# Kernel optimization log

Measured on AMD Instinct MI355X. Metric: run time of the kernel, lower is better.

## Reference

```python
import jax, jax.numpy as jnp
import numpy as np

N, E, DIN, DH, R = 50000, 1600000, 128, 128, 3


def setup_inputs() -> dict:
    key = jax.random.key(0)
    ks = jax.random.split(key, 32)
    inp = {}
    inp["x"] = jax.random.normal(ks[0], (N, DIN), jnp.float32)
    inp["h_prev"] = jax.random.normal(ks[1], (N, DH), jnp.float32)
    inp["edge_index"] = jax.random.randint(ks[2], (2, E), 0, N)
    inp["node_role"] = jax.random.randint(ks[3], (N,), 0, R)
    i = 4
    for name, din, has_b in (("xz", DIN, True), ("hz", DH, False), ("xr", DIN, True), ("hr", DH, False), ("xh", DIN, True), ("hh", DH, False)):
        inp[name + "_W"] = jax.random.normal(ks[i], (din, DH), jnp.float32) / np.float32(np.sqrt(din)); i += 1
        inp[name + "_Wg"] = jax.random.normal(ks[i], (R, DH), jnp.float32) * np.float32(0.1); i += 1
        inp[name + "_bg"] = jnp.zeros((R, DH), jnp.float32)
        inp[name + "_S"] = jax.random.normal(ks[i], (R, DH, DH), jnp.float32) / np.float32(np.sqrt(DH)); i += 1
        if has_b:
            inp[name + "_b"] = jnp.zeros((R, DH), jnp.float32)
    return inp


def _role_conv(x, W, Wg, bg, S, b, row, col, node_role):
    # x: [N, din] -> transformed features [N, DH]
    xt = x @ W
    r = node_role[row]                                  # role of source node per edge
    g = jax.nn.sigmoid(Wg[r] + bg[r])                   # [Etot, DH] role gate
    msg = xt[row] * g
    if b is not None:
        msg = msg + b[r]
    n = x.shape[0]
    summed = jax.ops.segment_sum(msg, col, num_segments=n)
    cnt = jax.ops.segment_sum(jnp.ones((row.shape[0],), xt.dtype), col, num_segments=n)
    aggr = summed / jnp.maximum(cnt, 1.0)[:, None]      # scatter_mean (self-loops ensure cnt>=1)
    # per-role self transform: out[i] = xt[i] @ S[role[i]] + aggr[i]
    out = aggr
    for nr in range(R):
        out = out + jnp.where((node_role == nr)[:, None], xt @ S[nr], jnp.float32(0.0))
    return jax.nn.relu(out)


def reference(x, edge_index, h_prev, node_role,
              xz_W, xz_Wg, xz_bg, xz_S, xz_b,
              hz_W, hz_Wg, hz_bg, hz_S,
              xr_W, xr_Wg, xr_bg, xr_S, xr_b,
              hr_W, hr_Wg, hr_bg, hr_S,
              xh_W, xh_Wg, xh_bg, xh_S, xh_b,
              hh_W, hh_Wg, hh_bg, hh_S):
    n = x.shape[0]
    loops = jnp.arange(n, dtype=edge_index.dtype)
    row = jnp.concatenate([edge_index[0], loops])       # add_self_loops appended at end
    col = jnp.concatenate([edge_index[1], loops])

    z = jax.nn.sigmoid(_role_conv(x, xz_W, xz_Wg, xz_bg, xz_S, xz_b, row, col, node_role)
                       + _role_conv(h_prev, hz_W, hz_Wg, hz_bg, hz_S, None, row, col, node_role))
    r = jax.nn.sigmoid(_role_conv(x, xr_W, xr_Wg, xr_bg, xr_S, xr_b, row, col, node_role)
                       + _role_conv(h_prev, hr_W, hr_Wg, hr_bg, hr_S, None, row, col, node_role))
    h_tilde = jnp.tanh(_role_conv(x, xh_W, xh_Wg, xh_bg, xh_S, xh_b, row, col, node_role)
                       + _role_conv(r * h_prev, hh_W, hh_Wg, hh_bg, hh_S, None, row, col, node_role))
    h_new = z * h_prev + (1.0 - z) * h_tilde
    return h_new
```

## Files before the change

### kernel.cpp

```cpp
#include <hip/hip_runtime.h>


typedef __bf16 bf16;
typedef __bf16 bf16x8 __attribute__((ext_vector_type(8)));
typedef float  f32x4  __attribute__((ext_vector_type(4)));
typedef float  f32x2  __attribute__((ext_vector_type(2)));
typedef unsigned char u8;

#define DH 128

__device__ __forceinline__ float sigmoidf_(float x) { return 1.0f / (1.0f + expf(-x)); }

__global__ __launch_bounds__(256) void hist_kernel(const int* __restrict__ ei, const int* __restrict__ role,
                                                   int* __restrict__ cnt3, int* __restrict__ rolecnt,
                                                   int E, int N)
{
  int i = blockIdx.x * 256 + threadIdx.x;
  int lane = threadIdx.x & 63;
  int r = (i < N) ? role[i] : -1;
  #pragma unroll
  for (int rr = 0; rr < 3; ++rr) {
    unsigned long long mask = __ballot(r == rr);
    if (lane == 0 && mask) atomicAdd(&rolecnt[rr], __popcll(mask));
  }
  if (i < E + N) {
    int src, dst;
    if (i < E) { src = ei[i]; dst = ei[E + i]; } else { src = i - E; dst = i - E; }
    int rs = (i < E) ? role[src] : r;
    if (i >= E) rs = role[i - E];
    atomicAdd(&cnt3[dst * 3 + rs], 1);
  }
}

__global__ __launch_bounds__(1024) void scan1_kernel(const int* __restrict__ cnt, int* __restrict__ off,
                                                     int* __restrict__ bsum, int n)
{
  __shared__ int wsum[16];
  int t = threadIdx.x, lane = t & 63, w = t >> 6;
  int idx = blockIdx.x * 1024 + t;
  int v = (idx < n) ? cnt[idx] : 0;
  int s = v;
  #pragma unroll
  for (int d = 1; d < 64; d <<= 1) { int u = __shfl_up(s, d); if (lane >= d) s += u; }
  if (lane == 63) wsum[w] = s;
  __syncthreads();
  if (w == 0 && lane < 16) {
    int ws = wsum[lane];
    #pragma unroll
    for (int d = 1; d < 16; d <<= 1) { int u = __shfl_up(ws, d); if (lane >= d) ws += u; }
    wsum[lane] = ws;
  }
  __syncthreads();
  int inc = ((w > 0) ? wsum[w - 1] : 0) + s;
  if (idx < n) off[idx + 1] = inc;
  if (t == 1023) bsum[blockIdx.x] = inc;
}

__global__ void scan2_kernel(int* __restrict__ bsum, int nb, const int* __restrict__ rolecnt,
                             int* __restrict__ rolefill, int* __restrict__ roleinfo)
{
  int lane = threadIdx.x;
  int carry = 0;
  for (int base = 0; base < nb; base += 64) {
    int v = (base + lane < nb) ? bsum[base + lane] : 0;
    int s = v;
    #pragma unroll
    for (int d = 1; d < 64; d <<= 1) { int u = __shfl_up(s, d); if (lane >= d) s += u; }
    if (base + lane < nb) bsum[base + lane] = carry + s - v;
    carry += __shfl(s, 63);
  }
  if (lane == 0) {
    int c0 = rolecnt[0], c1 = rolecnt[1], c2 = rolecnt[2];
    int s1 = (c0 + 255) & ~255;
    int s2 = s1 + ((c1 + 255) & ~255);
    int mp = s2 + ((c2 + 255) & ~255);
    rolefill[0] = 0; rolefill[1] = s1; rolefill[2] = s2;
    roleinfo[0] = s1; roleinfo[1] = s2;
    roleinfo[2] = c0;      roleinfo[3] = s1 - c0;
    roleinfo[4] = s1 + c1; roleinfo[5] = s2 - s1 - c1;
    roleinfo[6] = s2 + c2; roleinfo[7] = mp - s2 - c2;
  }
}

__global__ __launch_bounds__(1024) void scan3_kernel(int* __restrict__ off, int* __restrict__ fill,
                                                     const int* __restrict__ bsum, int n)
{
  int idx = blockIdx.x * 1024 + threadIdx.x;
  if (idx == 0) { off[0] = 0; fill[0] = 0; }
  if (idx < n) {
    int v = off[idx + 1] + bsum[blockIdx.x];
    off[idx + 1] = v;
    if (idx + 1 < n) fill[idx + 1] = v;
  }
}

__global__ __launch_bounds__(256) void scatter_kernel(const int* __restrict__ ei, const int* __restrict__ spos,
                                                      const int* __restrict__ roleinfo,
                                                      int* __restrict__ fill3, int* __restrict__ ssrc, int E, int N)
{
  int i = blockIdx.x * 256 + threadIdx.x;
  if (i >= E + N) return;
  int s1 = roleinfo[0], s2 = roleinfo[1];
  int src, dst;
  if (i < E) { src = ei[i]; dst = ei[E + i]; } else { src = i - E; dst = i - E; }
  int t = spos[src];
  int r = (t >= s2) ? 2 : (t >= s1) ? 1 : 0;
  int pz = atomicAdd(&fill3[dst * 3 + r], 1);
  ssrc[pz] = t;
}

__global__ __launch_bounds__(256) void permscatter_kernel(const int* __restrict__ role, int* __restrict__ rolefill,
                                                          int* __restrict__ spos, int* __restrict__ sposinv, int N)
{
  int i = blockIdx.x * 256 + threadIdx.x;
  int lane = threadIdx.x & 63;
  int r = (i < N) ? role[i] : -1;
  #pragma unroll
  for (int rr = 0; rr < 3; ++rr) {
    unsigned long long mask = __ballot(r == rr);
    if (!mask) continue;
    int base = 0;
    if (lane == 0) base = atomicAdd(&rolefill[rr], __popcll(mask));
    base = __shfl(base, 0);
    if (r == rr) {
      int rank = (int)__popcll(mask & ((1ull << lane) - 1ull));
      int pos = base + rank;
      spos[i] = pos;
      sposinv[pos] = i;
    }
  }
}

__global__ __launch_bounds__(256) void zeropad_kernel(const int* __restrict__ roleinfo,
                                                      bf16* __restrict__ Ax, bf16* __restrict__ Ah)
{
  int id = blockIdx.x * 256 + threadIdx.x;
  int a = id / 49152, rem = id % 49152;
  int gp = rem / 16384, r2 = rem % 16384;
  int rr = r2 >> 6, c = r2 & 63;
  int gs = roleinfo[2 + gp * 2], gl = roleinfo[3 + gp * 2];
  if (rr < gl) {
    int row = gs + rr;
    size_t unit = (size_t)(row >> 4) * 1024 + c * 16 + (row & 15);
    bf16x8 z = {};
    ((bf16x8*)(a == 0 ? Ax : Ah))[unit] = z;
  }
}

__global__ __launch_bounds__(256) void prep_xh_kernel(const float* __restrict__ x, const float* __restrict__ h,
                                                      const int* __restrict__ spos, u8* __restrict__ xq8,
                                                      bf16* __restrict__ Ax, bf16* __restrict__ Ah, int N)
{
  int g = blockIdx.x * 256 + threadIdx.x;
  if (g >= N * 32) return;
  int n = g >> 5, j = g & 31;
  int t = spos[n];
  const float* src = (j < 16) ? (x + (size_t)n * 128 + (j << 3))
                              : (h + (size_t)n * 128 + ((j - 16) << 3));
  float4 v0 = ((const float4*)src)[0];
  float4 v1 = ((const float4*)src)[1];
  int lo = __builtin_amdgcn_cvt_pk_fp8_f32(v0.x, v0.y, 0, false);
  lo = __builtin_amdgcn_cvt_pk_fp8_f32(v0.z, v0.w, lo, true);
  int hi = __builtin_amdgcn_cvt_pk_fp8_f32(v1.x, v1.y, 0, false);
  hi = __builtin_amdgcn_cvt_pk_fp8_f32(v1.z, v1.w, hi, true);
  *(int2*)(xq8 + (size_t)t * 256 + j * 8) = make_int2(lo, hi);
  bf16x8 o;
  o[0] = (bf16)v0.x; o[1] = (bf16)v0.y; o[2] = (bf16)v0.z; o[3] = (bf16)v0.w;
  o[4] = (bf16)v1.x; o[5] = (bf16)v1.y; o[6] = (bf16)v1.z; o[7] = (bf16)v1.w;
  size_t unit = (size_t)(t >> 4) * 1024 + (48 + (j & 15)) * 16 + (t & 15);
  ((bf16x8*)(j < 16 ? Ax : Ah))[unit] = o;
}

struct PrepW { const float* W[6]; const float* Wg[6]; const float* bg[6]; };
__global__ __launch_bounds__(256) void prep_wf_kernel(PrepW pw, bf16* __restrict__ Wf)
{
  int idx = blockIdx.x * 256 + threadIdx.x;
  if (idx >= 294912) return;
  int cv = idx / 49152, pos = idx % 49152;
  int ks4q = pos >> 10;
  int col = (pos >> 3) & 127, j = pos & 7;
  int k = (ks4q >> 2) * 32 + (ks4q & 3) * 8 + j;
  int r = k >> 7, kk = k & 127;
  float g = sigmoidf_(pw.Wg[cv][r * 128 + col] + pw.bg[cv][r * 128 + col]);
  Wf[idx] = (bf16)(pw.W[cv][kk * 128 + col] * g);
}

struct PrepP { const float* W[6]; const float* S[6]; };
__global__ __launch_bounds__(128) void prep_pf_kernel(PrepP pp, bf16* __restrict__ Pf)
{
  int b = blockIdx.x;
  int cv = b / 384, rem = b % 384;
  int r = rem >> 7, kp = rem & 127;
  int col = threadIdx.x;
  const float* W = pp.W[cv] + (size_t)kp * 128;
  const float* S = pp.S[cv] + (size_t)r * 16384;
  float sum = 0.f;
  #pragma unroll 4
  for (int j2 = 0; j2 < 128; ++j2) sum += W[j2] * S[j2 * 128 + col];
  size_t o = (size_t)(cv * 3 + r) * 16384 + ((size_t)(kp >> 3) * 128 + col) * 8 + (kp & 7);
  Pf[o] = (bf16)sum;
}

#define ACCUM16(U, d) do { f32x2 f_;                                                   \
  f_ = __builtin_amdgcn_cvt_pk_f32_fp8((d).x, false); U[0]  += f_[0]; U[1]  += f_[1];  \
  f_ = __builtin_amdgcn_cvt_pk_f32_fp8((d).x, true);  U[2]  += f_[0]; U[3]  += f_[1];  \
  f_ = __builtin_amdgcn_cvt_pk_f32_fp8((d).y, false); U[4]  += f_[0]; U[5]  += f_[1];  \
  f_ = __builtin_amdgcn_cvt_pk_f32_fp8((d).y, true);  U[6]  += f_[0]; U[7]  += f_[1];  \
  f_ = __builtin_amdgcn_cvt_pk_f32_fp8((d).z, false); U[8]  += f_[0]; U[9]  += f_[1];  \
  f_ = __builtin_amdgcn_cvt_pk_f32_fp8((d).z, true);  U[10] += f_[0]; U[11] += f_[1];  \
  f_ = __builtin_amdgcn_cvt_pk_f32_fp8((d).w, false); U[12] += f_[0]; U[13] += f_[1];  \
  f_ = __builtin_amdgcn_cvt_pk_f32_fp8((d).w, true);  U[14] += f_[0]; U[15] += f_[1];  \
} while (0)

#define ACCSEL16(d, p) do {                      \
  if ((p) < o1)      { ACCUM16(u0, d); }         \
  else if ((p) < o2) { ACCUM16(u1, d); }         \
  else               { ACCUM16(u2, d); }         \
} while (0)

__global__ __launch_bounds__(512) void gather_xh_kernel(
    const u8* __restrict__ xq8, const int* __restrict__ off3, const int* __restrict__ ssrc,
    const int* __restrict__ sposinv, bf16* __restrict__ Ax, bf16* __restrict__ Ah,
    float4* __restrict__ cntf)
{
  __shared__ alignas(16) bf16 lds[8][768];
  int w = threadIdx.x >> 6, lane = threadIdx.x & 63;
  int t0 = blockIdx.x * 8;
  int t = t0 + w;
  int node = sposinv[t];
  int qt = lane >> 4, ql = lane & 15;

  if (node >= 0) {
    int o0 = __builtin_amdgcn_readfirstlane(off3[node * 3]);
    int o1 = __builtin_amdgcn_readfirstlane(off3[node * 3 + 1]);
    int o2 = __builtin_amdgcn_readfirstlane(off3[node * 3 + 2]);
    int o3 = __builtin_amdgcn_readfirstlane(off3[node * 3 + 3]);
    float inv = 1.0f / (float)(o3 - o0);
    const u8* base = xq8 + ql * 16;

    float u0[16], u1[16], u2[16];
    #pragma unroll
    for (int k = 0; k < 16; ++k) { u0[k] = 0.f; u1[k] = 0.f; u2[k] = 0.f; }

    const int e = o3, emax = o3 - 1;
    for (int i = o0; i < e; i += 16) {
      int p0 = i + qt, p1 = p0 + 4, p2 = p0 + 8, p3 = p0 + 12;
      int t0i = ssrc[min(p0, emax)];
      int t1i = ssrc[min(p1, emax)];
      int t2i = ssrc[min(p2, emax)];
      int t3i = ssrc[min(p3, emax)];
      int4 d0 = make_int4(0, 0, 0, 0), d1 = d0, d2 = d0, d3 = d0;
      if (p0 < e) d0 = *(const int4*)(base + (size_t)t0i * 256);
      if (p1 < e) d1 = *(const int4*)(base + (size_t)t1i * 256);
      if (p2 < e) d2 = *(const int4*)(base + (size_t)t2i * 256);
      if (p3 < e) d3 = *(const int4*)(base + (size_t)t3i * 256);
      ACCSEL16(d0, p0);
      ACCSEL16(d1, p1);
      ACCSEL16(d2, p2);
      ACCSEL16(d3, p3);
    }

    #pragma unroll
    for (int k = 0; k < 16; ++k) {
      u0[k] += __shfl_xor(u0[k], 16); u0[k] += __shfl_xor(u0[k], 32);
      u1[k] += __shfl_xor(u1[k], 16); u1[k] += __shfl_xor(u1[k], 32);
      u2[k] += __shfl_xor(u2[k], 16); u2[k] += __shfl_xor(u2[k], 32);
    }
    if (qt == 0) {
      bf16x8 p0v, p1v;
      int sb0 = (ql < 8) ? (ql * 16) : (384 + (ql - 8) * 16);
      #pragma unroll
      for (int k = 0; k < 8; ++k) { p0v[k] = (bf16)(u0[k] * inv); p1v[k] = (bf16)(u0[8 + k] * inv); }
      *(bf16x8*)&lds[w][sb0] = p0v;
      *(bf16x8*)&lds[w][sb0 + 8] = p1v;
      #pragma unroll
      for (int k = 0; k < 8; ++k) { p0v[k] = (bf16)(u1[k] * inv); p1v[k] = (bf16)(u1[8 + k] * inv); }
      *(bf16x8*)&lds[w][sb0 + 128] = p0v;
      *(bf16x8*)&lds[w][sb0 + 136] = p1v;
      #pragma unroll
      for (int k = 0; k < 8; ++k) { p0v[k] = (bf16)(u2[k] * inv); p1v[k] = (bf16)(u2[8 + k] * inv); }
      *(bf16x8*)&lds[w][sb0 + 256] = p0v;
      *(bf16x8*)&lds[w][sb0 + 264] = p1v;
    }
    if (lane == 0)
      cntf[t] = make_float4((o1 - o0) * inv, (o2 - o1) * inv, (o3 - o2) * inv, (float)(o3 - o0));
  } else {
    if (lane < 48) {
      bf16x8 z = {};
      *(bf16x8*)&lds[w][lane * 16] = z;
      *(bf16x8*)&lds[w][lane * 16 + 8] = z;
    }
    if (lane == 0) cntf[t] = make_float4(0.f, 0.f, 0.f, 0.f);
  }

  __syncthreads();

  int tid = threadIdx.x;
  if (tid < 384) {
    int lc = tid >> 3, row = tid & 7;
    size_t unit = (size_t)(t0 >> 4) * 1024 + lc * 16 + (t0 & 15) + row;
    __builtin_nontemporal_store(*(const bf16x8*)&lds[row][lc * 8], (bf16x8*)Ax + unit);
    __builtin_nontemporal_store(*(const bf16x8*)&lds[row][384 + lc * 8], (bf16x8*)Ah + unit);
  }
}

#define ACCUM8(U, d) do { f32x2 f_;                                                  \
  f_ = __builtin_amdgcn_cvt_pk_f32_fp8((d).x, false); U[0] += f_[0]; U[1] += f_[1];  \
  f_ = __builtin_amdgcn_cvt_pk_f32_fp8((d).x, true);  U[2] += f_[0]; U[3] += f_[1];  \
  f_ = __builtin_amdgcn_cvt_pk_f32_fp8((d).y, false); U[4] += f_[0]; U[5] += f_[1];  \
  f_ = __builtin_amdgcn_cvt_pk_f32_fp8((d).y, true);  U[6] += f_[0]; U[7] += f_[1];  \
} while (0)

#define ACCSEL8(d, p) do {                      \
  if ((p) < o1)      { ACCUM8(v0, d); }         \
  else if ((p) < o2) { ACCUM8(v1, d); }         \
  else               { ACCUM8(v2, d); }         \
} while (0)

__global__ __launch_bounds__(512) void gather_q_kernel(
    const u8* __restrict__ q8, const int* __restrict__ off3, const int* __restrict__ ssrc,
    const int* __restrict__ sposinv, bf16* __restrict__ Aq)
{
  __shared__ alignas(16) bf16 lds[8][384];
  int w = threadIdx.x >> 6, lane = threadIdx.x & 63;
  int t0 = blockIdx.x * 8;
  int t = t0 + w;
  int node = sposinv[t];
  int qt = lane >> 4, ql = lane & 15;

  if (node >= 0) {
    int o0 = __builtin_amdgcn_readfirstlane(off3[node * 3]);
    int o1 = __builtin_amdgcn_readfirstlane(off3[node * 3 + 1]);
    int o2 = __builtin_amdgcn_readfirstlane(off3[node * 3 + 2]);
    int o3 = __builtin_amdgcn_readfirstlane(off3[node * 3 + 3]);
    float inv = 1.0f / (float)(o3 - o0);
    const u8* base = q8 + ql * 8;

    float v0[8], v1[8], v2[8];
    #pragma unroll
    for (int k = 0; k < 8; ++k) { v0[k] = 0.f; v1[k] = 0.f; v2[k] = 0.f; }

    const int e = o3, emax = o3 - 1;
    for (int i = o0; i < e; i += 16) {
      int p0 = i + qt, p1 = p0 + 4, p2 = p0 + 8, p3 = p0 + 12;
      int t0i = ssrc[min(p0, emax)];
      int t1i = ssrc[min(p1, emax)];
      int t2i = ssrc[min(p2, emax)];
      int t3i = ssrc[min(p3, emax)];
      int2 d0 = make_int2(0, 0), d1 = d0, d2 = d0, d3 = d0;
      if (p0 < e) d0 = *(const int2*)(base + (size_t)t0i * 128);
      if (p1 < e) d1 = *(const int2*)(base + (size_t)t1i * 128);
      if (p2 < e) d2 = *(const int2*)(base + (size_t)t2i * 128);
      if (p3 < e) d3 = *(const int2*)(base + (size_t)t3i * 128);
      ACCSEL8(d0, p0);
      ACCSEL8(d1, p1);
      ACCSEL8(d2, p2);
      ACCSEL8(d3, p3);
    }

    #pragma unroll
    for (int k = 0; k < 8; ++k) {
      v0[k] += __shfl_xor(v0[k], 16); v0[k] += __shfl_xor(v0[k], 32);
      v1[k] += __shfl_xor(v1[k], 16); v1[k] += __shfl_xor(v1[k], 32);
      v2[k] += __shfl_xor(v2[k], 16); v2[k] += __shfl_xor(v2[k], 32);
    }
    if (qt == 0) {
      bf16x8 pk;
      #pragma unroll
      for (int k = 0; k < 8; ++k) pk[k] = (bf16)(v0[k] * inv);
      *(bf16x8*)&lds[w][ql * 8] = pk;
      #pragma unroll
      for (int k = 0; k < 8; ++k) pk[k] = (bf16)(v1[k] * inv);
      *(bf16x8*)&lds[w][128 + ql * 8] = pk;
      #pragma unroll
      for (int k = 0; k < 8; ++k) pk[k] = (bf16)(v2[k] * inv);
      *(bf16x8*)&lds[w][256 + ql * 8] = pk;
    }
  } else {
    if (lane < 48) {
      bf16x8 z = {};
      *(bf16x8*)&lds[w][lane * 8] = z;
    }
  }

  __syncthreads();

  int tid = threadIdx.x;
  if (tid < 384) {
    int lc = tid >> 3, row = tid & 7;
    size_t unit = (size_t)(t0 >> 4) * 1024 + lc * 16 + (t0 & 15) + row;
    __builtin_nontemporal_store(*(const bf16x8*)&lds[row][lc * 8], (bf16x8*)Aq + unit);
  }
}

struct GArgs {
  const bf16* Ap[5];
  const bf16* wf[5];
  const bf16* pf[5];
  bf16* out[5];
  const float* bias[5];
};

__global__ __launch_bounds__(256) void gemm_kernel(GArgs ga, const float4* __restrict__ cntf,
                                                   const int* __restrict__ roleinfo)
{
  const int cv = blockIdx.y;
  const bf16* __restrict__ Ap = ga.Ap[cv];
  const bf16* __restrict__ wf = ga.wf[cv];
  const bf16* __restrict__ pf = ga.pf[cv];
  bf16* __restrict__ out = ga.out[cv];
  const float* __restrict__ bias = ga.bias[cv];

  const int w = threadIdx.x >> 6, lane = threadIdx.x & 63;
  const int q = lane >> 4, l = lane & 15;
  const int rb0 = blockIdx.x * 16 + w * 4;
  const int row0 = blockIdx.x * 256;
  const int s1 = roleinfo[0], s2 = roleinfo[1];
  const int role = (row0 >= s2) ? 2 : (row0 >= s1) ? 1 : 0;
  const int laneoff = q * 128 + l;

  f32x4 acc[4][8];
  #pragma unroll
  for (int j = 0; j < 4; ++j)
    #pragma unroll
    for (int ct = 0; ct < 8; ++ct)
      #pragma unroll
      for (int k = 0; k < 4; ++k) acc[j][ct][k] = 0.f;

  const bf16x8* A0 = (const bf16x8*)Ap + (size_t)rb0 * 1024 + lane;
  const bf16x8* WF = (const bf16x8*)wf + laneoff;
  const bf16x8* PF = (const bf16x8*)pf + role * 2048 + laneoff;

  #pragma unroll 2
  for (int ks = 0; ks < 16; ++ks) {
    const bf16x8* bp = (ks < 12) ? (WF + ks * 512) : (PF + (ks - 12) * 512);
    bf16x8 a0 = A0[ks * 64];
    bf16x8 a1 = A0[1024 + ks * 64];
    bf16x8 a2 = A0[2048 + ks * 64];
    bf16x8 a3 = A0[3072 + ks * 64];
    #pragma unroll
    for (int ct = 0; ct < 8; ++ct) {
      bf16x8 b = bp[ct * 16];
      acc[0][ct] = __builtin_amdgcn_mfma_f32_16x16x32_bf16(a0, b, acc[0][ct], 0, 0, 0);
      acc[1][ct] = __builtin_amdgcn_mfma_f32_16x16x32_bf16(a1, b, acc[1][ct], 0, 0, 0);
      acc[2][ct] = __builtin_amdgcn_mfma_f32_16x16x32_bf16(a2, b, acc[2][ct], 0, 0, 0);
      acc[3][ct] = __builtin_amdgcn_mfma_f32_16x16x32_bf16(a3, b, acc[3][ct], 0, 0, 0);
    }
  }

  const bool hb = (bias != nullptr);
  #pragma unroll
  for (int j = 0; j < 4; ++j) {
    int rb = rb0 + j;
    float4 cfs[4];
    if (hb) {
      #pragma unroll
      for (int reg = 0; reg < 4; ++reg) cfs[reg] = cntf[rb * 16 + q * 4 + reg];
    }
    #pragma unroll
    for (int ct = 0; ct < 8; ++ct) {
      int col = ct * 16 + l;
      float b0 = 0, b1 = 0, b2 = 0;
      if (hb) { b0 = bias[col]; b1 = bias[128 + col]; b2 = bias[256 + col]; }
      #pragma unroll
      for (int reg = 0; reg < 4; ++reg) {
        int t = rb * 16 + q * 4 + reg;
        float v = acc[j][ct][reg];
        if (hb) v += cfs[reg].x * b0 + cfs[reg].y * b1 + cfs[reg].z * b2;
        out[(size_t)t * 128 + col] = (bf16)fmaxf(v, 0.f);
      }
    }
  }
}

__global__ __launch_bounds__(256) void combine1_kernel(
    const bf16* __restrict__ o0, const bf16* __restrict__ o1,
    const bf16* __restrict__ o2, const bf16* __restrict__ o3,
    const float* __restrict__ h, const int* __restrict__ spos,
    float* __restrict__ zbuf, u8* __restrict__ q8, bf16* __restrict__ Aq, int N)
{
  int g = blockIdx.x * 256 + threadIdx.x;
  if (g >= N * 16) return;
  int n = g >> 4, o = g & 15;
  int t = spos[n];
  size_t tb = (size_t)t * 16 + o;
  bf16x8 a0 = ((const bf16x8*)o0)[tb];
  bf16x8 a1 = ((const bf16x8*)o1)[tb];
  bf16x8 a2 = ((const bf16x8*)o2)[tb];
  bf16x8 a3 = ((const bf16x8*)o3)[tb];
  size_t nb = (size_t)n * 16 + o;
  float4 h0 = ((const float4*)h)[nb * 2];
  float4 h1 = ((const float4*)h)[nb * 2 + 1];
  float hv[8] = {h0.x, h0.y, h0.z, h0.w, h1.x, h1.y, h1.z, h1.w};
  float zv[8], qv[8];
  bf16x8 qb;
  #pragma unroll
  for (int j = 0; j < 8; ++j) {
    zv[j] = sigmoidf_((float)a0[j] + (float)a1[j]);
    qv[j] = sigmoidf_((float)a2[j] + (float)a3[j]) * hv[j];
    qb[j] = (bf16)qv[j];
  }
  ((float4*)zbuf)[nb * 2]     = make_float4(zv[0], zv[1], zv[2], zv[3]);
  ((float4*)zbuf)[nb * 2 + 1] = make_float4(zv[4], zv[5], zv[6], zv[7]);
  int lo = __builtin_amdgcn_cvt_pk_fp8_f32(qv[0], qv[1], 0, false);
  lo = __builtin_amdgcn_cvt_pk_fp8_f32(qv[2], qv[3], lo, true);
  int hi = __builtin_amdgcn_cvt_pk_fp8_f32(qv[4], qv[5], 0, false);
  hi = __builtin_amdgcn_cvt_pk_fp8_f32(qv[6], qv[7], hi, true);
  *(int2*)(q8 + (size_t)t * 128 + o * 8) = make_int2(lo, hi);
  size_t unit = (size_t)(t >> 4) * 1024 + (48 + o) * 16 + (t & 15);
  ((bf16x8*)Aq)[unit] = qb;
}

__global__ __launch_bounds__(256) void combine2_kernel(
    const float* __restrict__ zbuf, const bf16* __restrict__ o4, const bf16* __restrict__ o5,
    const float* __restrict__ h, const int* __restrict__ spos, float* __restrict__ out, int N)
{
  int g = blockIdx.x * 256 + threadIdx.x;
  if (g >= N * 16) return;
  int n = g >> 4, o = g & 15;
  int t = spos[n];
  size_t tb = (size_t)t * 16 + o;
  bf16x8 a = ((const bf16x8*)o4)[tb];
  bf16x8 b = ((const bf16x8*)o5)[tb];
  size_t nb = (size_t)n * 16 + o;
  float4 z0 = ((const float4*)zbuf)[nb * 2];
  float4 z1 = ((const float4*)zbuf)[nb * 2 + 1];
  float4 h0 = ((const float4*)h)[nb * 2];
  float4 h1 = ((const float4*)h)[nb * 2 + 1];
  float zv[8] = {z0.x, z0.y, z0.z, z0.w, z1.x, z1.y, z1.z, z1.w};
  float hv[8] = {h0.x, h0.y, h0.z, h0.w, h1.x, h1.y, h1.z, h1.w};
  float ov[8];
  #pragma unroll
  for (int j = 0; j < 8; ++j)
    ov[j] = zv[j] * hv[j] + (1.f - zv[j]) * tanhf((float)a[j] + (float)b[j]);
  ((float4*)out)[nb * 2]     = make_float4(ov[0], ov[1], ov[2], ov[3]);
  ((float4*)out)[nb * 2 + 1] = make_float4(ov[4], ov[5], ov[6], ov[7]);
}

extern "C" void kernel_launch(void* const* d_in, const int* in_sizes, int n_in,
                              void* d_out, int out_size, void* d_ws, size_t ws_size,
                              hipStream_t stream)
{
  (void)n_in; (void)out_size; (void)ws_size;
  const float* x    = (const float*)d_in[0];
  const float* h    = (const float*)d_in[1];
  const int*   ei   = (const int*)d_in[2];
  const int*   role = (const int*)d_in[3];
  const int N = in_sizes[0] / DH;
  const int E = in_sizes[2] / 2;
  const int Etot = E + N;
  const int rows_pad = ((N + 765) + 255) & ~255;
  const int gx = rows_pad / 256;
  const int n3 = N * 3;
  const int nb3 = (n3 + 1023) / 1024;

  static const int Wi[6]  = {4, 9, 13, 18, 22, 27};
  static const int Wgi[6] = {5, 10, 14, 19, 23, 28};
  static const int bgi[6] = {6, 11, 15, 20, 24, 29};
  static const int Si[6]  = {7, 12, 16, 21, 25, 30};

  char* p = (char*)d_ws;
  auto alloc = [&](size_t bytes) -> char* {
    char* r = p;
    p += (bytes + 255) & ~(size_t)255;
    return r;
  };

  bf16* Ax = (bf16*)alloc((size_t)rows_pad * 512 * 2);
  bf16* Ah = (bf16*)alloc((size_t)rows_pad * 512 * 2);
  bf16* Aq = Ax;
  u8* xq8  = (u8*)alloc((size_t)rows_pad * 256);
  u8* q8   = (u8*)alloc((size_t)rows_pad * 128);
  bf16* outs[6];
  for (int c = 0; c < 5; ++c) outs[c] = (bf16*)alloc((size_t)rows_pad * 128 * 2);
  outs[5] = outs[0];
  float* zbuf = (float*)alloc((size_t)N * 128 * 4);
  float4* cntf = (float4*)alloc((size_t)rows_pad * 16);
  bf16* Wf = (bf16*)alloc((size_t)6 * 49152 * 2);
  bf16* Pf = (bf16*)alloc((size_t)18 * 16384 * 2);
  int* cnt3  = (int*)alloc((size_t)n3 * 4);
  int* off3  = (int*)alloc((size_t)(n3 + 1) * 4);
  int* fill3 = (int*)alloc((size_t)n3 * 4);
  int* bsum  = (int*)alloc((size_t)(nb3 + 1) * 4);
  int* ssrc  = (int*)alloc((size_t)Etot * 4);
  int* spos  = (int*)alloc((size_t)N * 4);
  int* sposinv = (int*)alloc((size_t)rows_pad * 4);
  int* rolecnt  = (int*)alloc(64);
  int* rolefill = (int*)alloc(64);
  int* roleinfo = (int*)alloc(64);

  hipMemsetAsync(cnt3, 0, (size_t)n3 * 4, stream);
  hipMemsetAsync(rolecnt, 0, 16, stream);
  hipMemsetAsync(sposinv, 0xFF, (size_t)rows_pad * 4, stream);

  int egrid = (Etot + 255) / 256;
  int ngrid = (N + 255) / 256;
  hist_kernel<<<egrid, 256, 0, stream>>>(ei, role, cnt3, rolecnt, E, N);
  scan1_kernel<<<nb3, 1024, 0, stream>>>(cnt3, off3, bsum, n3);
  scan2_kernel<<<1, 64, 0, stream>>>(bsum, nb3, rolecnt, rolefill, roleinfo);
  scan3_kernel<<<nb3, 1024, 0, stream>>>(off3, fill3, bsum, n3);
  permscatter_kernel<<<ngrid, 256, 0, stream>>>(role, rolefill, spos, sposinv, N);
  scatter_kernel<<<egrid, 256, 0, stream>>>(ei, spos, roleinfo, fill3, ssrc, E, N);
  zeropad_kernel<<<384, 256, 0, stream>>>(roleinfo, Ax, Ah);

  prep_xh_kernel<<<(N * 32 + 255) / 256, 256, 0, stream>>>(x, h, spos, xq8, Ax, Ah, N);

  PrepW pw;
  for (int c = 0; c < 6; ++c) {
    pw.W[c] = (const float*)d_in[Wi[c]];
    pw.Wg[c] = (const float*)d_in[Wgi[c]];
    pw.bg[c] = (const float*)d_in[bgi[c]];
  }
  prep_wf_kernel<<<1152, 256, 0, stream>>>(pw, Wf);
  PrepP pp;
  for (int c = 0; c < 6; ++c) { pp.W[c] = (const float*)d_in[Wi[c]]; pp.S[c] = (const float*)d_in[Si[c]]; }
  prep_pf_kernel<<<2304, 128, 0, stream>>>(pp, Pf);

  gather_xh_kernel<<<rows_pad / 8, 512, 0, stream>>>(xq8, off3, ssrc, sposinv, Ax, Ah, cntf);

  GArgs g0;
  { int cvs[5] = {0, 2, 4, 1, 3};
    static const int bi2[5] = {8, 17, 26, -1, -1};
    const bf16* Apts[5] = {Ax, Ax, Ax, Ah, Ah};
    for (int k = 0; k < 5; ++k) {
      int c = cvs[k];
      g0.Ap[k] = Apts[k];
      g0.wf[k] = Wf + (size_t)c * 49152;
      g0.pf[k] = Pf + (size_t)c * 3 * 16384;
      g0.out[k] = outs[c];
      g0.bias[k] = (bi2[k] >= 0) ? (const float*)d_in[bi2[k]] : nullptr;
    } }
  gemm_kernel<<<dim3(gx, 5), 256, 0, stream>>>(g0, cntf, roleinfo);

  combine1_kernel<<<(N * 16 + 255) / 256, 256, 0, stream>>>(outs[0], outs[1], outs[2], outs[3],
                                                            h, spos, zbuf, q8, Aq, N);

  gather_q_kernel<<<rows_pad / 8, 512, 0, stream>>>(q8, off3, ssrc, sposinv, Aq);

  GArgs g2 = {};
  g2.Ap[0] = Aq;
  g2.wf[0] = Wf + (size_t)5 * 49152;
  g2.pf[0] = Pf + (size_t)5 * 3 * 16384;
  g2.out[0] = outs[5];
  g2.bias[0] = nullptr;
  gemm_kernel<<<dim3(gx, 1), 256, 0, stream>>>(g2, cntf, roleinfo);

  combine2_kernel<<<(N * 16 + 255) / 256, 256, 0, stream>>>(zbuf, outs[4], outs[5], h, spos,
                                                            (float*)d_out, N);
}
```

Measured before the change: 730.0 us.

## Replace random CSR scatter with two-pass bucketed partition then local scatter

```diff
diff --git a/kernel.cpp b/kernel.cpp
--- a/kernel.cpp
+++ b/kernel.cpp
@@ -94,19 +94,69 @@
   }
 }
 
-__global__ __launch_bounds__(256) void scatter_kernel(const int* __restrict__ ei, const int* __restrict__ spos,
-                                                      const int* __restrict__ roleinfo,
-                                                      int* __restrict__ fill3, int* __restrict__ ssrc, int E, int N)
-{
-  int i = blockIdx.x * 256 + threadIdx.x;
-  if (i >= E + N) return;
-  int s1 = roleinfo[0], s2 = roleinfo[1];
-  int src, dst;
-  if (i < E) { src = ei[i]; dst = ei[E + i]; } else { src = i - E; dst = i - E; }
-  int t = spos[src];
-  int r = (t >= s2) ? 2 : (t >= s1) ? 1 : 0;
-  int pz = atomicAdd(&fill3[dst * 3 + r], 1);
-  ssrc[pz] = t;
+__global__ void bucketinit_kernel(const int* __restrict__ off3, int* __restrict__ bucketfill,
+                                  int NB, int W, int N)
+{
+  int b = blockIdx.x * 256 + threadIdx.x;
+  if (b < NB) {
+    int d = min(b * W, N);
+    bucketfill[b] = off3[d * 3];
+  }
+}
+
+__global__ __launch_bounds__(256) void partition_kernel(
+    const int* __restrict__ ei, const int* __restrict__ spos,
+    const int* __restrict__ roleinfo, int* __restrict__ bucketfill,
+    int2* __restrict__ recs, int E, int N, int shiftB)
+{
+  __shared__ int lcnt[256], lbase[256];
+  const int base = blockIdx.x * 4096;
+  const int s1 = roleinfo[0], s2 = roleinfo[1];
+  lcnt[threadIdx.x] = 0;
+  __syncthreads();
+  int myb[16], mybin[16], myt[16];
+  #pragma unroll
+  for (int k = 0; k < 16; ++k) {
+    int i = base + k * 256 + threadIdx.x;
+    myb[k] = -1;
+    if (i < E + N) {
+      int src, dst;
+      if (i < E) { src = ei[i]; dst = ei[E + i]; } else { src = i - E; dst = i - E; }
+      int t = spos[src];
+      int r = (t >= s2) ? 2 : (t >= s1) ? 1 : 0;
+      myb[k] = dst >> shiftB;
+      mybin[k] = dst * 3 + r;
+      myt[k] = t;
+      atomicAdd(&lcnt[myb[k]], 1);
+    }
+  }
+  __syncthreads();
+  int c = lcnt[threadIdx.x];
+  lbase[threadIdx.x] = (c > 0) ? atomicAdd(&bucketfill[threadIdx.x], c) : 0;
+  __syncthreads();
+  lcnt[threadIdx.x] = 0;
+  __syncthreads();
+  #pragma unroll
+  for (int k = 0; k < 16; ++k) {
+    if (myb[k] >= 0) {
+      int slot = atomicAdd(&lcnt[myb[k]], 1);
+      recs[lbase[myb[k]] + slot] = make_int2(mybin[k], myt[k]);
+    }
+  }
+}
+
+__global__ __launch_bounds__(1024) void binscatter_kernel(
+    const int2* __restrict__ recs, const int* __restrict__ off3,
+    int* __restrict__ fill3, int* __restrict__ ssrc, int W, int N)
+{
+  int b = blockIdx.x;
+  int d0 = min(b * W, N), d1 = min((b + 1) * W, N);
+  int s = off3[d0 * 3], e = off3[d1 * 3];
+  for (int i = s + threadIdx.x; i < e; i += 1024) {
+    int2 rec = recs[i];
+    int pz = atomicAdd(&fill3[rec.x], 1);
+    ssrc[pz] = rec.y;
+  }
 }
 
 __global__ __launch_bounds__(256) void permscatter_kernel(const int* __restrict__ role, int* __restrict__ rolefill,
@@ -554,6 +604,11 @@
   const int n3 = N * 3;
   const int nb3 = (n3 + 1023) / 1024;
 
+  int shiftB = 8;
+  while (((N - 1) >> shiftB) >= 256) ++shiftB;
+  const int W = 1 << shiftB;
+  const int NB = (N + W - 1) >> shiftB;
+
   static const int Wi[6]  = {4, 9, 13, 18, 22, 27};
   static const int Wgi[6] = {5, 10, 14, 19, 23, 28};
   static const int bgi[6] = {6, 11, 15, 20, 24, 29};
@@ -583,11 +638,13 @@
   int* fill3 = (int*)alloc((size_t)n3 * 4);
   int* bsum  = (int*)alloc((size_t)(nb3 + 1) * 4);
   int* ssrc  = (int*)alloc((size_t)Etot * 4);
+  int2* recs = (int2*)alloc((size_t)Etot * 8);
   int* spos  = (int*)alloc((size_t)N * 4);
   int* sposinv = (int*)alloc((size_t)rows_pad * 4);
   int* rolecnt  = (int*)alloc(64);
   int* rolefill = (int*)alloc(64);
   int* roleinfo = (int*)alloc(64);
+  int* bucketfill = (int*)alloc((size_t)(NB + 1) * 4);
 
   hipMemsetAsync(cnt3, 0, (size_t)n3 * 4, stream);
   hipMemsetAsync(rolecnt, 0, 16, stream);
@@ -600,7 +657,10 @@
   scan2_kernel<<<1, 64, 0, stream>>>(bsum, nb3, rolecnt, rolefill, roleinfo);
   scan3_kernel<<<nb3, 1024, 0, stream>>>(off3, fill3, bsum, n3);
   permscatter_kernel<<<ngrid, 256, 0, stream>>>(role, rolefill, spos, sposinv, N);
-  scatter_kernel<<<egrid, 256, 0, stream>>>(ei, spos, roleinfo, fill3, ssrc, E, N);
+  bucketinit_kernel<<<1, 256, 0, stream>>>(off3, bucketfill, NB, W, N);
+  partition_kernel<<<(Etot + 4095) / 4096, 256, 0, stream>>>(ei, spos, roleinfo, bucketfill,
+                                                             recs, E, N, shiftB);
+  binscatter_kernel<<<NB, 1024, 0, stream>>>(recs, off3, fill3, ssrc, W, N);
   zeropad_kernel<<<384, 256, 0, stream>>>(roleinfo, Ax, Ah);
 
   prep_xh_kernel<<<(N * 32 + 255) / 256, 256, 0, stream>>>(x, h, spos, xq8, Ax, Ah, N);
```

Measured after the change: 704.2 us. 3.5% less time.
